# Optimization experiments

Hardware: AMD Instinct MI355X
Metric: run time of the kernel (lower is better)

The kernel has to match this reference:

```python
import jax, jax.numpy as jnp
import numpy as np


def cubic_feats(x):
    # x: [B, d] -> [B, d + (d^2+d)/2 + d]
    d = x.shape[1]
    iu0, iu1 = jnp.triu_indices(d)  # upper-triangular incl. diagonal, static for fixed d
    quad = x[:, iu0] * x[:, iu1]    # [B, (d^2+d)/2], avoids materializing [B,d,d]
    return jnp.concatenate([x, quad, x ** 3], axis=-1)


def setup_inputs() -> dict:
    key = jax.random.key(0)
    ks = jax.random.split(key, 5)
    d_in, hidden, d_out, batch = 512, 512, 256, 512
    dc_in = d_in + (d_in ** 2 + d_in) // 2 + d_in      # 132352
    dc_h = hidden + (hidden ** 2 + hidden) // 2 + hidden
    s0 = 1.0 / np.sqrt(dc_in)
    s1 = 1.0 / np.sqrt(dc_h)
    return {
        "x": jax.random.normal(ks[0], (batch, d_in), dtype=jnp.float32),
        "W0": jax.random.normal(ks[1], (hidden, dc_in), dtype=jnp.float32) * s0,
        "b0": jax.random.normal(ks[2], (hidden,), dtype=jnp.float32) * s0,
        "W1": jax.random.normal(ks[3], (d_out, dc_h), dtype=jnp.float32) * s1,
        "b1": jax.random.normal(ks[4], (d_out,), dtype=jnp.float32) * s1,
    }


def reference(x, W0, b0, W1, b1):
    # layer 0: cubic feature expansion + linear
    h = cubic_feats(x) @ W0.T + b0          # [B, hidden]
    # layer 1 (output): expansion on hidden activations + linear
    out = cubic_feats(h) @ W1.T + b1        # [B, dim_out]
    return out
```

## Files before the change

kernel.cpp:

```cpp
#include <hip/hip_runtime.h>
#include <hip/hip_bf16.h>
#include <stdint.h>


#define D_IN      512
#define BATCH     512
#define K_TOT     132352
#define QUAD_BASE 512
#define CUBE_BASE 131840
#define BN        128
#define BK        64

typedef __attribute__((ext_vector_type(8))) __bf16 bf16x8;
typedef __attribute__((ext_vector_type(4))) float  f32x4;

__device__ __forceinline__ bf16x8 pack8(float a0, float a1, float a2, float a3,
                                        float a4, float a5, float a6, float a7) {
    bf16x8 r;
    r[0] = (__bf16)a0; r[1] = (__bf16)a1; r[2] = (__bf16)a2; r[3] = (__bf16)a3;
    r[4] = (__bf16)a4; r[5] = (__bf16)a5; r[6] = (__bf16)a6; r[7] = (__bf16)a7;
    return r;
}

__device__ __forceinline__ void decode_quad(int q, int& oi, int& oj) {
    float s = sqrtf((float)(1050625 - 8 * q));
    int i = (int)((1025.0f - s) * 0.5f);
    i = i < 0 ? 0 : (i > 511 ? 511 : i);
    while (i < 511 && (i + 1) * (1025 - (i + 1)) / 2 <= q) ++i;
    while (i > 0 && i * (1025 - i) / 2 > q) --i;
    oi = i; oj = i + (q - i * (1025 - i) / 2);
}

__device__ __forceinline__ void stage_A(const float* __restrict__ X,
                                        uint8_t* __restrict__ Ab,
                                        int kw, int tid) {
    const int c  = tid & 7;
    const int r0 = tid >> 3;
    const int k  = kw + c * 8;
    uint8_t* const wp0 = Ab + (size_t)r0 * 128 + (uint32_t)((c ^ (r0 & 7)) * 16);
    const float* const xrow = X + (size_t)r0 * D_IN;

    if (k < QUAD_BASE) {
        #pragma unroll 2
        for (int p = 0; p < 4; ++p) {
            const float* row = xrow + (size_t)p * (128 * D_IN);
            float4 a = *(const float4*)(row + k);
            float4 b = *(const float4*)(row + k + 4);
            *(bf16x8*)(wp0 + p * 16384) = pack8(a.x, a.y, a.z, a.w, b.x, b.y, b.z, b.w);
        }
    } else if (k >= CUBE_BASE) {
        const int tt = k - CUBE_BASE;
        #pragma unroll 2
        for (int p = 0; p < 4; ++p) {
            const float* row = xrow + (size_t)p * (128 * D_IN);
            float4 a = *(const float4*)(row + tt);
            float4 b = *(const float4*)(row + tt + 4);
            *(bf16x8*)(wp0 + p * 16384) = pack8(
                a.x * a.x * a.x, a.y * a.y * a.y, a.z * a.z * a.z, a.w * a.w * a.w,
                b.x * b.x * b.x, b.y * b.y * b.y, b.z * b.z * b.z, b.w * b.w * b.w);
        }
    } else {
        int i0, j0; decode_quad(k - QUAD_BASE, i0, j0);
        if (j0 <= 504) {
            #pragma unroll 2
            for (int p = 0; p < 4; ++p) {
                const float* row = xrow + (size_t)p * (128 * D_IN);
                const float xi = row[i0];
                float4 a = *(const float4*)(row + j0);
                float4 b = *(const float4*)(row + j0 + 4);
                *(bf16x8*)(wp0 + p * 16384) = pack8(
                    xi * a.x, xi * a.y, xi * a.z, xi * a.w,
                    xi * b.x, xi * b.y, xi * b.z, xi * b.w);
            }
        } else {
            #pragma unroll 2
            for (int p = 0; p < 4; ++p) {
                const float* row = xrow + (size_t)p * (128 * D_IN);
                int i = i0, j = j0;
                float xi = row[i];
                float v[8];
                #pragma unroll
                for (int e = 0; e < 8; ++e) {
                    v[e] = xi * row[j];
                    ++j;
                    if (j == 512) { ++i; j = i; xi = row[i]; }
                }
                *(bf16x8*)(wp0 + p * 16384) = pack8(v[0], v[1], v[2], v[3],
                                                    v[4], v[5], v[6], v[7]);
            }
        }
    }
}

__global__ __launch_bounds__(1024, 1) void gemm_fused(
    const float* __restrict__ X,
    const float* __restrict__ W,
    float* __restrict__ C, int ldc,
    const float* __restrict__ bias, int split_steps)
{
    extern __shared__ uint8_t smem[];
    const int tid  = threadIdx.x;
    const int lane = tid & 63;
    const int wave = tid >> 6;
    const int wm   = wave >> 1;
    const int wn   = wave & 1;
    const int n0   = blockIdx.x * BN;
    const int ks   = blockIdx.y;

    const int kbeg = ks * split_steps * BK;
    const int kend = min(K_TOT, kbeg + split_steps * BK);
    if (kbeg >= kend) return;
    const int nt = (kend - kbeg) / BK;

    const int brow   = tid >> 3;
    const int bchunk = tid & 7;
    const float* const wsrc = W + (size_t)(n0 + brow) * K_TOT + bchunk * 8;
    const uint32_t boff = (uint32_t)brow * 128 + (uint32_t)((bchunk ^ (brow & 7)) * 16);

    {
        float4 w0 = *(const float4*)(wsrc + kbeg);
        float4 w1 = *(const float4*)(wsrc + kbeg + 4);
        stage_A(X, smem, kbeg, tid);
        *(bf16x8*)(smem + 131072 + boff) =
            pack8(w0.x, w0.y, w0.z, w0.w, w1.x, w1.y, w1.z, w1.w);
    }
    __syncthreads();

    f32x4 acc[4][4] = {};
    const int fr = lane & 15;
    const int h  = lane >> 4;
    uint32_t aoff[4], boffr[4];
    #pragma unroll
    for (int i = 0; i < 4; ++i) {
        aoff[i]  = (uint32_t)(wm * 64 + i * 16 + fr) * 128;
        boffr[i] = (uint32_t)(wn * 64 + i * 16 + fr) * 128;
    }
    const uint32_t cs0 = (uint32_t)((h ^ (lane & 7)) * 16);
    const uint32_t cs1 = cs0 ^ 64u;

    for (int t = 0; t < nt; ++t) {
        const uint32_t cur = (uint32_t)(t & 1);
        const uint8_t* const Ab = smem + cur * 65536u;
        const uint8_t* const Bb = smem + 131072u + cur * 16384u;
        const bool pre = (t + 1 < nt);
        const int kkn = kbeg + (t + 1) * BK;

        float4 nw0, nw1;
        if (pre) {
            nw0 = *(const float4*)(wsrc + kkn);
            nw1 = *(const float4*)(wsrc + kkn + 4);
        }

        __builtin_amdgcn_s_setprio(1);
        #pragma unroll
        for (int s = 0; s < 2; ++s) {
            const uint32_t cs = s ? cs1 : cs0;
            bf16x8 a[4];
            #pragma unroll
            for (int mf = 0; mf < 4; ++mf)
                a[mf] = *(const bf16x8*)(Ab + aoff[mf] + cs);
            #pragma unroll
            for (int nf = 0; nf < 4; ++nf) {
                bf16x8 b = *(const bf16x8*)(Bb + boffr[nf] + cs);
                #pragma unroll
                for (int mf = 0; mf < 4; ++mf)
                    acc[mf][nf] = __builtin_amdgcn_mfma_f32_16x16x32_bf16(a[mf], b, acc[mf][nf], 0, 0, 0);
            }
        }
        __builtin_amdgcn_s_setprio(0);

        if (pre) {
            stage_A(X, smem + (cur ^ 1u) * 65536u, kkn, tid);
            *(bf16x8*)(smem + 131072u + (cur ^ 1u) * 16384u + boff) =
                pack8(nw0.x, nw0.y, nw0.z, nw0.w, nw1.x, nw1.y, nw1.z, nw1.w);
        }
        __syncthreads();
    }

    const bool dob = (ks == 0);
    const int rbase = wm * 64 + (lane >> 4) * 4;
    const int cbase = n0 + wn * 64 + (lane & 15);
    #pragma unroll
    for (int nf = 0; nf < 4; ++nf) {
        const int col = cbase + nf * 16;
        const float bv = dob ? bias[col] : 0.0f;
        #pragma unroll
        for (int mf = 0; mf < 4; ++mf) {
            const int row = rbase + mf * 16;
            #pragma unroll
            for (int r = 0; r < 4; ++r)
                unsafeAtomicAdd(&C[(size_t)(row + r) * ldc + col], acc[mf][nf][r] + bv);
        }
    }
}

extern "C" void kernel_launch(void* const* d_in, const int* in_sizes, int n_in,
                              void* d_out, int out_size, void* d_ws, size_t ws_size,
                              hipStream_t stream)
{
    const float* x  = (const float*)d_in[0];
    const float* W0 = (const float*)d_in[1];
    const float* b0 = (const float*)d_in[2];
    const float* W1 = (const float*)d_in[3];
    const float* b1 = (const float*)d_in[4];
    float* out = (float*)d_out;

    float* hbuf = (float*)d_ws;
    const size_t hbytes = (size_t)BATCH * 512 * 4;

    static int lds_set = 0;
    if (!lds_set) {
        hipFuncSetAttribute((const void*)gemm_fused,
                            hipFuncAttributeMaxDynamicSharedMemorySize, 163840);
        lds_set = 1;
    }

    hipMemsetAsync(hbuf, 0, hbytes, stream);
    hipMemsetAsync(out, 0, (size_t)out_size * 4, stream);

    const int TS = K_TOT / BK;

    {
        const int ss = 33;
        const int gy = (TS + ss - 1) / ss;
        gemm_fused<<<dim3(512 / BN, gy), 1024, 163840, stream>>>(
            x, W0, hbuf, 512, b0, ss);
    }
    {
        const int ss = 17;
        const int gy = (TS + ss - 1) / ss;
        gemm_fused<<<dim3(256 / BN, gy), 1024, 163840, stream>>>(
            hbuf, W1, out, 256, b1, ss);
    }
}
```

Baseline: 353.8 us.

## Split A staging into early global loads and later LDS writes to overlap MFMA

A-tile feature generation is split into an issue phase, where the global loads of x values go into registers before the MFMA loop, and a write phase after the MFMA loop that does the multiplies, converts to bf16 and stores to LDS. This hides global-load latency behind the matrix math, as was already done for the W tile. Mode selection moves to per-k-tile granularity, and a new branch-free path covers tiles that cross a single row boundary of the triangle. The risk is much higher register pressure from holding 40-plus floats across the MFMA loop at 1024 threads per block, which could cause spills.

After: 1.147 ms. 224% more time.

```diff
diff --git a/kernel.cpp b/kernel.cpp
--- a/kernel.cpp
+++ b/kernel.cpp
@@ -31,63 +31,142 @@
     oi = i; oj = i + (q - i * (1025 - i) / 2);
 }
 
-__device__ __forceinline__ void stage_A(const float* __restrict__ X,
-                                        uint8_t* __restrict__ Ab,
-                                        int kw, int tid) {
+struct Stg {
+    float4 va[4], vb[4];
+    float  xi[4], xi1[4];
+    int    s1;
+    int    mode;
+};
+
+__device__ __forceinline__ void stage_issue(const float* __restrict__ X,
+                                            int kw, int tid, Stg& st)
+{
     const int c  = tid & 7;
     const int r0 = tid >> 3;
-    const int k  = kw + c * 8;
+    const float* const xr = X + (size_t)r0 * D_IN;
+    const int k = kw + c * 8;
+
+    if (kw < QUAD_BASE) {
+        st.mode = 0;
+        #pragma unroll
+        for (int p = 0; p < 4; ++p) {
+            const float* row = xr + (size_t)p * (128 * D_IN);
+            st.va[p] = *(const float4*)(row + k);
+            st.vb[p] = *(const float4*)(row + k + 4);
+        }
+    } else if (kw >= CUBE_BASE) {
+        st.mode = 1;
+        const int tt = k - CUBE_BASE;
+        #pragma unroll
+        for (int p = 0; p < 4; ++p) {
+            const float* row = xr + (size_t)p * (128 * D_IN);
+            st.va[p] = *(const float4*)(row + tt);
+            st.vb[p] = *(const float4*)(row + tt + 4);
+        }
+    } else {
+        const int qw = kw - QUAD_BASE;
+        int iw, jw; decode_quad(qw, iw, jw);
+        if (jw + 63 <= 511) {
+            st.mode = 2;
+            const int j0 = jw + c * 8;
+            #pragma unroll
+            for (int p = 0; p < 4; ++p) {
+                const float* row = xr + (size_t)p * (128 * D_IN);
+                st.xi[p] = row[iw];
+                st.va[p] = *(const float4*)(row + j0);
+                st.vb[p] = *(const float4*)(row + j0 + 4);
+            }
+        } else {
+            int ie, je; decode_quad(qw + 63, ie, je);
+            if (ie <= 504) {
+                st.mode = 3;
+                int i0, j0; decode_quad(qw + c * 8, i0, j0);
+                const int s1   = 512 - j0;
+                const int off1 = i0 + j0 - 511;
+                st.s1 = s1;
+                const int x0 = (0 < s1 ? j0 : off1) + 0;
+                const int x1 = (1 < s1 ? j0 : off1) + 1;
+                const int x2 = (2 < s1 ? j0 : off1) + 2;
+                const int x3 = (3 < s1 ? j0 : off1) + 3;
+                const int x4 = (4 < s1 ? j0 : off1) + 4;
+                const int x5 = (5 < s1 ? j0 : off1) + 5;
+                const int x6 = (6 < s1 ? j0 : off1) + 6;
+                const int x7 = (7 < s1 ? j0 : off1) + 7;
+                #pragma unroll
+                for (int p = 0; p < 4; ++p) {
+                    const float* row = xr + (size_t)p * (128 * D_IN);
+                    st.xi[p]  = row[i0];
+                    st.xi1[p] = row[i0 + 1];
+                    st.va[p].x = row[x0]; st.va[p].y = row[x1];
+                    st.va[p].z = row[x2]; st.va[p].w = row[x3];
+                    st.vb[p].x = row[x4]; st.vb[p].y = row[x5];
+                    st.vb[p].z = row[x6]; st.vb[p].w = row[x7];
+                }
+            } else {
+                st.mode = 4;
+            }
+        }
+    }
+}
+
+__device__ __forceinline__ void stage_write(uint8_t* __restrict__ Ab,
+                                            const float* __restrict__ X,
+                                            int kw, int tid, const Stg& st)
+{
+    const int c  = tid & 7;
+    const int r0 = tid >> 3;
     uint8_t* const wp0 = Ab + (size_t)r0 * 128 + (uint32_t)((c ^ (r0 & 7)) * 16);
-    const float* const xrow = X + (size_t)r0 * D_IN;
-
-    if (k < QUAD_BASE) {
-        #pragma unroll 2
-        for (int p = 0; p < 4; ++p) {
-            const float* row = xrow + (size_t)p * (128 * D_IN);
-            float4 a = *(const float4*)(row + k);
-            float4 b = *(const float4*)(row + k + 4);
-            *(bf16x8*)(wp0 + p * 16384) = pack8(a.x, a.y, a.z, a.w, b.x, b.y, b.z, b.w);
-        }
-    } else if (k >= CUBE_BASE) {
-        const int tt = k - CUBE_BASE;
-        #pragma unroll 2
-        for (int p = 0; p < 4; ++p) {
-            const float* row = xrow + (size_t)p * (128 * D_IN);
-            float4 a = *(const float4*)(row + tt);
-            float4 b = *(const float4*)(row + tt + 4);
+
+    if (st.mode == 0) {
+        #pragma unroll
+        for (int p = 0; p < 4; ++p)
+            *(bf16x8*)(wp0 + p * 16384) = pack8(
+                st.va[p].x, st.va[p].y, st.va[p].z, st.va[p].w,
+                st.vb[p].x, st.vb[p].y, st.vb[p].z, st.vb[p].w);
+    } else if (st.mode == 1) {
+        #pragma unroll
+        for (int p = 0; p < 4; ++p) {
+            float4 a = st.va[p], b = st.vb[p];
             *(bf16x8*)(wp0 + p * 16384) = pack8(
                 a.x * a.x * a.x, a.y * a.y * a.y, a.z * a.z * a.z, a.w * a.w * a.w,
                 b.x * b.x * b.x, b.y * b.y * b.y, b.z * b.z * b.z, b.w * b.w * b.w);
         }
+    } else if (st.mode == 2) {
+        #pragma unroll
+        for (int p = 0; p < 4; ++p) {
+            const float xi = st.xi[p];
+            *(bf16x8*)(wp0 + p * 16384) = pack8(
+                xi * st.va[p].x, xi * st.va[p].y, xi * st.va[p].z, xi * st.va[p].w,
+                xi * st.vb[p].x, xi * st.vb[p].y, xi * st.vb[p].z, xi * st.vb[p].w);
+        }
+    } else if (st.mode == 3) {
+        const int s1 = st.s1;
+        #pragma unroll
+        for (int p = 0; p < 4; ++p) {
+            const float xa = st.xi[p], xb = st.xi1[p];
+            *(bf16x8*)(wp0 + p * 16384) = pack8(
+                (0 < s1 ? xa : xb) * st.va[p].x, (1 < s1 ? xa : xb) * st.va[p].y,
+                (2 < s1 ? xa : xb) * st.va[p].z, (3 < s1 ? xa : xb) * st.va[p].w,
+                (4 < s1 ? xa : xb) * st.vb[p].x, (5 < s1 ? xa : xb) * st.vb[p].y,
+                (6 < s1 ? xa : xb) * st.vb[p].z, (7 < s1 ? xa : xb) * st.vb[p].w);
+        }
     } else {
+        const int k = kw + c * 8;
         int i0, j0; decode_quad(k - QUAD_BASE, i0, j0);
-        if (j0 <= 504) {
-            #pragma unroll 2
-            for (int p = 0; p < 4; ++p) {
-                const float* row = xrow + (size_t)p * (128 * D_IN);
-                const float xi = row[i0];
-                float4 a = *(const float4*)(row + j0);
-                float4 b = *(const float4*)(row + j0 + 4);
-                *(bf16x8*)(wp0 + p * 16384) = pack8(
-                    xi * a.x, xi * a.y, xi * a.z, xi * a.w,
-                    xi * b.x, xi * b.y, xi * b.z, xi * b.w);
+        #pragma unroll 1
+        for (int p = 0; p < 4; ++p) {
+            const float* row = X + (size_t)(r0 + p * 128) * D_IN;
+            int i = i0, j = j0;
+            float xi = row[i];
+            float v[8];
+            #pragma unroll
+            for (int e = 0; e < 8; ++e) {
+                v[e] = xi * row[j];
+                ++j;
+                if (e < 7 && j == 512) { ++i; j = i; xi = row[i]; }
             }
-        } else {
-            #pragma unroll 2
-            for (int p = 0; p < 4; ++p) {
-                const float* row = xrow + (size_t)p * (128 * D_IN);
-                int i = i0, j = j0;
-                float xi = row[i];
-                float v[8];
-                #pragma unroll
-                for (int e = 0; e < 8; ++e) {
-                    v[e] = xi * row[j];
-                    ++j;
-                    if (j == 512) { ++i; j = i; xi = row[i]; }
-                }
-                *(bf16x8*)(wp0 + p * 16384) = pack8(v[0], v[1], v[2], v[3],
-                                                    v[4], v[5], v[6], v[7]);
-            }
+            *(bf16x8*)(wp0 + p * 16384) = pack8(v[0], v[1], v[2], v[3],
+                                                v[4], v[5], v[6], v[7]);
         }
     }
 }
@@ -117,10 +196,12 @@
     const float* const wsrc = W + (size_t)(n0 + brow) * K_TOT + bchunk * 8;
     const uint32_t boff = (uint32_t)brow * 128 + (uint32_t)((bchunk ^ (brow & 7)) * 16);
 
+    Stg st;
+    stage_issue(X, kbeg, tid, st);
     {
         float4 w0 = *(const float4*)(wsrc + kbeg);
         float4 w1 = *(const float4*)(wsrc + kbeg + 4);
-        stage_A(X, smem, kbeg, tid);
+        stage_write(smem, X, kbeg, tid, st);
         *(bf16x8*)(smem + 131072 + boff) =
             pack8(w0.x, w0.y, w0.z, w0.w, w1.x, w1.y, w1.z, w1.w);
     }
@@ -147,6 +228,7 @@
 
         float4 nw0, nw1;
         if (pre) {
+            stage_issue(X, kkn, tid, st);
             nw0 = *(const float4*)(wsrc + kkn);
             nw1 = *(const float4*)(wsrc + kkn + 4);
         }
@@ -170,7 +252,7 @@
         __builtin_amdgcn_s_setprio(0);
 
         if (pre) {
-            stage_A(X, smem + (cur ^ 1u) * 65536u, kkn, tid);
+            stage_write(smem + (cur ^ 1u) * 65536u, X, kkn, tid, st);
             *(bf16x8*)(smem + 131072u + (cur ^ 1u) * 16384u + boff) =
                 pack8(nw0.x, nw0.y, nw0.z, nw0.w, nw1.x, nw1.y, nw1.z, nw1.w);
         }
```

## Prefetch W two steps ahead, make quad decode wave-uniform, relax barrier waitcnt

Applied to the files above, without the earlier changes.

The W tile is now prefetched two k-steps ahead in registers, and the end-of-iteration barrier is replaced by a manual s_waitcnt lgkmcnt(0) / vmcnt(2) plus s_barrier, so the outstanding W loads stay in flight across the barrier. Quad-feature staging now branches on the wave-uniform tile start rather than per-thread k, and the row-wrap case is handled with a branch-free two-row select. The goal is to hide global latency on W and cut divergence in the quad decode. In exchange it uses more registers, and the hand-written vmcnt count depends on compiler load ordering, which could cause hazards if the compiler reorders loads.

New measurement: 782.4 us. +121.1%, slower.

```diff
diff --git a/kernel.cpp b/kernel.cpp
--- a/kernel.cpp
+++ b/kernel.cpp
@@ -38,21 +38,21 @@
     const int r0 = tid >> 3;
     const int k  = kw + c * 8;
     uint8_t* const wp0 = Ab + (size_t)r0 * 128 + (uint32_t)((c ^ (r0 & 7)) * 16);
-    const float* const xrow = X + (size_t)r0 * D_IN;
-
-    if (k < QUAD_BASE) {
+    const float* const xr = X + (size_t)r0 * D_IN;
+
+    if (kw < QUAD_BASE) {
         #pragma unroll 2
         for (int p = 0; p < 4; ++p) {
-            const float* row = xrow + (size_t)p * (128 * D_IN);
+            const float* row = xr + (size_t)p * (128 * D_IN);
             float4 a = *(const float4*)(row + k);
             float4 b = *(const float4*)(row + k + 4);
             *(bf16x8*)(wp0 + p * 16384) = pack8(a.x, a.y, a.z, a.w, b.x, b.y, b.z, b.w);
         }
-    } else if (k >= CUBE_BASE) {
+    } else if (kw >= CUBE_BASE) {
         const int tt = k - CUBE_BASE;
         #pragma unroll 2
         for (int p = 0; p < 4; ++p) {
-            const float* row = xrow + (size_t)p * (128 * D_IN);
+            const float* row = xr + (size_t)p * (128 * D_IN);
             float4 a = *(const float4*)(row + tt);
             float4 b = *(const float4*)(row + tt + 4);
             *(bf16x8*)(wp0 + p * 16384) = pack8(
@@ -60,12 +60,14 @@
                 b.x * b.x * b.x, b.y * b.y * b.y, b.z * b.z * b.z, b.w * b.w * b.w);
         }
     } else {
-        int i0, j0; decode_quad(k - QUAD_BASE, i0, j0);
-        if (j0 <= 504) {
+        const int qw = kw - QUAD_BASE;
+        int iw, jw; decode_quad(qw, iw, jw);
+        if (jw + 63 <= 511) {
+            const int j0 = jw + c * 8;
             #pragma unroll 2
             for (int p = 0; p < 4; ++p) {
-                const float* row = xrow + (size_t)p * (128 * D_IN);
-                const float xi = row[i0];
+                const float* row = xr + (size_t)p * (128 * D_IN);
+                const float xi = row[iw];
                 float4 a = *(const float4*)(row + j0);
                 float4 b = *(const float4*)(row + j0 + 4);
                 *(bf16x8*)(wp0 + p * 16384) = pack8(
@@ -73,20 +75,42 @@
                     xi * b.x, xi * b.y, xi * b.z, xi * b.w);
             }
         } else {
-            #pragma unroll 2
-            for (int p = 0; p < 4; ++p) {
-                const float* row = xrow + (size_t)p * (128 * D_IN);
-                int i = i0, j = j0;
-                float xi = row[i];
-                float v[8];
+            int ie, je; decode_quad(qw + 63, ie, je);
+            if (ie <= 504) {
+                int i0, j0; decode_quad(qw + c * 8, i0, j0);
+                const int s1   = 512 - j0;
+                const int off1 = i0 + j0 - 511;
+                int xx[8];
                 #pragma unroll
-                for (int e = 0; e < 8; ++e) {
-                    v[e] = xi * row[j];
-                    ++j;
-                    if (j == 512) { ++i; j = i; xi = row[i]; }
+                for (int e = 0; e < 8; ++e) xx[e] = (e < s1 ? j0 : off1) + e;
+                #pragma unroll 2
+                for (int p = 0; p < 4; ++p) {
+                    const float* row = xr + (size_t)p * (128 * D_IN);
+                    const float xa = row[i0];
+                    const float xb = row[i0 + 1];
+                    *(bf16x8*)(wp0 + p * 16384) = pack8(
+                        (0 < s1 ? xa : xb) * row[xx[0]], (1 < s1 ? xa : xb) * row[xx[1]],
+                        (2 < s1 ? xa : xb) * row[xx[2]], (3 < s1 ? xa : xb) * row[xx[3]],
+                        (4 < s1 ? xa : xb) * row[xx[4]], (5 < s1 ? xa : xb) * row[xx[5]],
+                        (6 < s1 ? xa : xb) * row[xx[6]], (7 < s1 ? xa : xb) * row[xx[7]]);
                 }
-                *(bf16x8*)(wp0 + p * 16384) = pack8(v[0], v[1], v[2], v[3],
-                                                    v[4], v[5], v[6], v[7]);
+            } else {
+                int i0, j0; decode_quad(qw + c * 8, i0, j0);
+                #pragma unroll 1
+                for (int p = 0; p < 4; ++p) {
+                    const float* row = xr + (size_t)p * (128 * D_IN);
+                    int i = i0, j = j0;
+                    float xi = row[i];
+                    float v[8];
+                    #pragma unroll
+                    for (int e = 0; e < 8; ++e) {
+                        v[e] = xi * row[j];
+                        ++j;
+                        if (e < 7 && j == 512) { ++i; j = i; xi = row[i]; }
+                    }
+                    *(bf16x8*)(wp0 + p * 16384) = pack8(v[0], v[1], v[2], v[3],
+                                                        v[4], v[5], v[6], v[7]);
+                }
             }
         }
     }
@@ -117,12 +141,17 @@
     const float* const wsrc = W + (size_t)(n0 + brow) * K_TOT + bchunk * 8;
     const uint32_t boff = (uint32_t)brow * 128 + (uint32_t)((bchunk ^ (brow & 7)) * 16);
 
+    stage_A(X, smem, kbeg, tid);
     {
         float4 w0 = *(const float4*)(wsrc + kbeg);
         float4 w1 = *(const float4*)(wsrc + kbeg + 4);
-        stage_A(X, smem, kbeg, tid);
         *(bf16x8*)(smem + 131072 + boff) =
             pack8(w0.x, w0.y, w0.z, w0.w, w1.x, w1.y, w1.z, w1.w);
+    }
+    float4 nwA0 = {}, nwA1 = {};
+    if (nt > 1) {
+        nwA0 = *(const float4*)(wsrc + kbeg + BK);
+        nwA1 = *(const float4*)(wsrc + kbeg + BK + 4);
     }
     __syncthreads();
 
@@ -142,13 +171,13 @@
         const uint32_t cur = (uint32_t)(t & 1);
         const uint8_t* const Ab = smem + cur * 65536u;
         const uint8_t* const Bb = smem + 131072u + cur * 16384u;
-        const bool pre = (t + 1 < nt);
-        const int kkn = kbeg + (t + 1) * BK;
-
-        float4 nw0, nw1;
-        if (pre) {
-            nw0 = *(const float4*)(wsrc + kkn);
-            nw1 = *(const float4*)(wsrc + kkn + 4);
+        const bool pre  = (t + 1 < nt);
+        const bool pre2 = (t + 2 < nt);
+
+        float4 nwB0 = {}, nwB1 = {};
+        if (pre2) {
+            nwB0 = *(const float4*)(wsrc + kbeg + (t + 2) * BK);
+            nwB1 = *(const float4*)(wsrc + kbeg + (t + 2) * BK + 4);
         }
 
         __builtin_amdgcn_s_setprio(1);
@@ -170,11 +199,17 @@
         __builtin_amdgcn_s_setprio(0);
 
         if (pre) {
-            stage_A(X, smem + (cur ^ 1u) * 65536u, kkn, tid);
+            stage_A(X, smem + (cur ^ 1u) * 65536u, kbeg + (t + 1) * BK, tid);
             *(bf16x8*)(smem + 131072u + (cur ^ 1u) * 16384u + boff) =
-                pack8(nw0.x, nw0.y, nw0.z, nw0.w, nw1.x, nw1.y, nw1.z, nw1.w);
-        }
-        __syncthreads();
+                pack8(nwA0.x, nwA0.y, nwA0.z, nwA0.w, nwA1.x, nwA1.y, nwA1.z, nwA1.w);
+            nwA0 = nwB0; nwA1 = nwB1;
+        }
+
+        asm volatile("s_waitcnt lgkmcnt(0)" ::: "memory");
+        asm volatile("s_waitcnt vmcnt(2)" ::: "memory");
+        __builtin_amdgcn_sched_barrier(0);
+        __builtin_amdgcn_s_barrier();
+        asm volatile("" ::: "memory");
     }
 
     const bool dob = (ks == 0);
```

## Split M into 256-row tiles with 512-thread blocks and single-buffered LDS

Applied to the files above, without the earlier changes.

Blocks now cover 256 rows of the batch instead of all 512, with 512 threads and static single-buffered shared memory (48KB), so up to four blocks fit per CU. Grid x doubles to cover both M halves. The register-prefetched double buffer is removed in favour of stage-then-sync-then-compute, so latency hiding now comes from co-resident blocks rather than intra-block pipelining. The quad decode is now done once per 64-wide k window when the window does not cross a row boundary, with per-chunk decode only in the crossing case. X rows are now expanded twice, once per M half.

Result: slower. 537.7 us (+52.0%).

```diff
diff --git a/kernel.cpp b/kernel.cpp
--- a/kernel.cpp
+++ b/kernel.cpp
@@ -8,6 +8,7 @@
 #define K_TOT     132352
 #define QUAD_BASE 512
 #define CUBE_BASE 131840
+#define BM        256
 #define BN        128
 #define BK        64
 
@@ -31,51 +32,54 @@
     oi = i; oj = i + (q - i * (1025 - i) / 2);
 }
 
-__device__ __forceinline__ void stage_A(const float* __restrict__ X,
+__device__ __forceinline__ void stage_A(const float* __restrict__ X, int m0,
                                         uint8_t* __restrict__ Ab,
                                         int kw, int tid) {
     const int c  = tid & 7;
     const int r0 = tid >> 3;
     const int k  = kw + c * 8;
     uint8_t* const wp0 = Ab + (size_t)r0 * 128 + (uint32_t)((c ^ (r0 & 7)) * 16);
-    const float* const xrow = X + (size_t)r0 * D_IN;
-
-    if (k < QUAD_BASE) {
+    const float* const xr = X + (size_t)(m0 + r0) * D_IN;
+
+    if (kw < QUAD_BASE) {
         #pragma unroll 2
         for (int p = 0; p < 4; ++p) {
-            const float* row = xrow + (size_t)p * (128 * D_IN);
+            const float* row = xr + (size_t)p * (64 * D_IN);
             float4 a = *(const float4*)(row + k);
             float4 b = *(const float4*)(row + k + 4);
-            *(bf16x8*)(wp0 + p * 16384) = pack8(a.x, a.y, a.z, a.w, b.x, b.y, b.z, b.w);
-        }
-    } else if (k >= CUBE_BASE) {
+            *(bf16x8*)(wp0 + p * 8192) = pack8(a.x, a.y, a.z, a.w, b.x, b.y, b.z, b.w);
+        }
+    } else if (kw >= CUBE_BASE) {
         const int tt = k - CUBE_BASE;
         #pragma unroll 2
         for (int p = 0; p < 4; ++p) {
-            const float* row = xrow + (size_t)p * (128 * D_IN);
+            const float* row = xr + (size_t)p * (64 * D_IN);
             float4 a = *(const float4*)(row + tt);
             float4 b = *(const float4*)(row + tt + 4);
-            *(bf16x8*)(wp0 + p * 16384) = pack8(
+            *(bf16x8*)(wp0 + p * 8192) = pack8(
                 a.x * a.x * a.x, a.y * a.y * a.y, a.z * a.z * a.z, a.w * a.w * a.w,
                 b.x * b.x * b.x, b.y * b.y * b.y, b.z * b.z * b.z, b.w * b.w * b.w);
         }
     } else {
-        int i0, j0; decode_quad(k - QUAD_BASE, i0, j0);
-        if (j0 <= 504) {
+        const int qw = kw - QUAD_BASE;
+        int iw, jw; decode_quad(qw, iw, jw);
+        if (jw + 63 <= 511) {
+            const int j0 = jw + c * 8;
             #pragma unroll 2
             for (int p = 0; p < 4; ++p) {
-                const float* row = xrow + (size_t)p * (128 * D_IN);
-                const float xi = row[i0];
+                const float* row = xr + (size_t)p * (64 * D_IN);
+                const float xi = row[iw];
                 float4 a = *(const float4*)(row + j0);
                 float4 b = *(const float4*)(row + j0 + 4);
-                *(bf16x8*)(wp0 + p * 16384) = pack8(
+                *(bf16x8*)(wp0 + p * 8192) = pack8(
                     xi * a.x, xi * a.y, xi * a.z, xi * a.w,
                     xi * b.x, xi * b.y, xi * b.z, xi * b.w);
             }
         } else {
-            #pragma unroll 2
+            int i0, j0; decode_quad(qw + c * 8, i0, j0);
+            #pragma unroll 1
             for (int p = 0; p < 4; ++p) {
-                const float* row = xrow + (size_t)p * (128 * D_IN);
+                const float* row = xr + (size_t)p * (64 * D_IN);
                 int i = i0, j = j0;
                 float xi = row[i];
                 float v[8];
@@ -83,28 +87,31 @@
                 for (int e = 0; e < 8; ++e) {
                     v[e] = xi * row[j];
                     ++j;
-                    if (j == 512) { ++i; j = i; xi = row[i]; }
+                    if (e < 7 && j == 512) { ++i; j = i; xi = row[i]; }
                 }
-                *(bf16x8*)(wp0 + p * 16384) = pack8(v[0], v[1], v[2], v[3],
-                                                    v[4], v[5], v[6], v[7]);
+                *(bf16x8*)(wp0 + p * 8192) = pack8(v[0], v[1], v[2], v[3],
+                                                   v[4], v[5], v[6], v[7]);
             }
         }
     }
 }
 
-__global__ __launch_bounds__(1024, 1) void gemm_fused(
+__global__ __launch_bounds__(512, 4) void gemm_fused(
     const float* __restrict__ X,
     const float* __restrict__ W,
     float* __restrict__ C, int ldc,
     const float* __restrict__ bias, int split_steps)
 {
-    extern __shared__ uint8_t smem[];
+    __shared__ uint8_t Asm[BM * 128];
+    __shared__ uint8_t Bsm[BN * 128];
+
     const int tid  = threadIdx.x;
     const int lane = tid & 63;
     const int wave = tid >> 6;
     const int wm   = wave >> 1;
     const int wn   = wave & 1;
-    const int n0   = blockIdx.x * BN;
+    const int m0   = (blockIdx.x & 1) * BM;
+    const int n0   = (blockIdx.x >> 1) * BN;
     const int ks   = blockIdx.y;
 
     const int kbeg = ks * split_steps * BK;
@@ -112,19 +119,13 @@
     if (kbeg >= kend) return;
     const int nt = (kend - kbeg) / BK;
 
-    const int brow   = tid >> 3;
-    const int bchunk = tid & 7;
-    const float* const wsrc = W + (size_t)(n0 + brow) * K_TOT + bchunk * 8;
-    const uint32_t boff = (uint32_t)brow * 128 + (uint32_t)((bchunk ^ (brow & 7)) * 16);
-
-    {
-        float4 w0 = *(const float4*)(wsrc + kbeg);
-        float4 w1 = *(const float4*)(wsrc + kbeg + 4);
-        stage_A(X, smem, kbeg, tid);
-        *(bf16x8*)(smem + 131072 + boff) =
-            pack8(w0.x, w0.y, w0.z, w0.w, w1.x, w1.y, w1.z, w1.w);
-    }
-    __syncthreads();
+    const int brow = tid >> 2;
+    const int bq   = tid & 3;
+    const float* const wsrc = W + (size_t)(n0 + brow) * K_TOT + bq * 16;
+    uint8_t* const bw0 = Bsm + (size_t)brow * 128
+                       + (uint32_t)(((2 * bq)     ^ (brow & 7)) * 16);
+    uint8_t* const bw1 = Bsm + (size_t)brow * 128
+                       + (uint32_t)(((2 * bq + 1) ^ (brow & 7)) * 16);
 
     f32x4 acc[4][4] = {};
     const int fr = lane & 15;
@@ -139,17 +140,19 @@
     const uint32_t cs1 = cs0 ^ 64u;
 
     for (int t = 0; t < nt; ++t) {
-        const uint32_t cur = (uint32_t)(t & 1);
-        const uint8_t* const Ab = smem + cur * 65536u;
-        const uint8_t* const Bb = smem + 131072u + cur * 16384u;
-        const bool pre = (t + 1 < nt);
-        const int kkn = kbeg + (t + 1) * BK;
-
-        float4 nw0, nw1;
-        if (pre) {
-            nw0 = *(const float4*)(wsrc + kkn);
-            nw1 = *(const float4*)(wsrc + kkn + 4);
-        }
+        const int kk = kbeg + t * BK;
+
+        stage_A(X, m0, Asm, kk, tid);
+        {
+            const float* wp = wsrc + kk;
+            float4 w0 = *(const float4*)(wp);
+            float4 w1 = *(const float4*)(wp + 4);
+            float4 w2 = *(const float4*)(wp + 8);
+            float4 w3 = *(const float4*)(wp + 12);
+            *(bf16x8*)bw0 = pack8(w0.x, w0.y, w0.z, w0.w, w1.x, w1.y, w1.z, w1.w);
+            *(bf16x8*)bw1 = pack8(w2.x, w2.y, w2.z, w2.w, w3.x, w3.y, w3.z, w3.w);
+        }
+        __syncthreads();
 
         __builtin_amdgcn_s_setprio(1);
         #pragma unroll
@@ -158,27 +161,21 @@
             bf16x8 a[4];
             #pragma unroll
             for (int mf = 0; mf < 4; ++mf)
-                a[mf] = *(const bf16x8*)(Ab + aoff[mf] + cs);
+                a[mf] = *(const bf16x8*)(Asm + aoff[mf] + cs);
             #pragma unroll
             for (int nf = 0; nf < 4; ++nf) {
-                bf16x8 b = *(const bf16x8*)(Bb + boffr[nf] + cs);
+                bf16x8 b = *(const bf16x8*)(Bsm + boffr[nf] + cs);
                 #pragma unroll
                 for (int mf = 0; mf < 4; ++mf)
                     acc[mf][nf] = __builtin_amdgcn_mfma_f32_16x16x32_bf16(a[mf], b, acc[mf][nf], 0, 0, 0);
             }
         }
         __builtin_amdgcn_s_setprio(0);
-
-        if (pre) {
-            stage_A(X, smem + (cur ^ 1u) * 65536u, kkn, tid);
-            *(bf16x8*)(smem + 131072u + (cur ^ 1u) * 16384u + boff) =
-                pack8(nw0.x, nw0.y, nw0.z, nw0.w, nw1.x, nw1.y, nw1.z, nw1.w);
-        }
         __syncthreads();
     }
 
     const bool dob = (ks == 0);
-    const int rbase = wm * 64 + (lane >> 4) * 4;
+    const int rbase = m0 + wm * 64 + (lane >> 4) * 4;
     const int cbase = n0 + wn * 64 + (lane & 15);
     #pragma unroll
     for (int nf = 0; nf < 4; ++nf) {
@@ -208,13 +205,6 @@
     float* hbuf = (float*)d_ws;
     const size_t hbytes = (size_t)BATCH * 512 * 4;
 
-    static int lds_set = 0;
-    if (!lds_set) {
-        hipFuncSetAttribute((const void*)gemm_fused,
-                            hipFuncAttributeMaxDynamicSharedMemorySize, 163840);
-        lds_set = 1;
-    }
-
     hipMemsetAsync(hbuf, 0, hbytes, stream);
     hipMemsetAsync(out, 0, (size_t)out_size * 4, stream);
 
@@ -223,13 +213,13 @@
     {
         const int ss = 33;
         const int gy = (TS + ss - 1) / ss;
-        gemm_fused<<<dim3(512 / BN, gy), 1024, 163840, stream>>>(
+        gemm_fused<<<dim3(8, gy), 512, 0, stream>>>(
             x, W0, hbuf, 512, b0, ss);
     }
     {
         const int ss = 17;
         const int gy = (TS + ss - 1) / ss;
-        gemm_fused<<<dim3(256 / BN, gy), 1024, 163840, stream>>>(
+        gemm_fused<<<dim3(4, gy), 512, 0, stream>>>(
             hbuf, W1, out, 256, b1, ss);
     }
 }
```
